# Kernel tuning notes

Hardware: AMD Instinct MI355X
Metric: run time of the kernel (lower is better)

Reference implementation:

```python
import jax, jax.numpy as jnp
import numpy as np

B, ES, HS, NL, NOUT, T = 16384, 64, 64, 3, 2, 128


def setup_inputs() -> dict:
    key = jax.random.key(0)
    ks = jax.random.split(key, 9)
    k = 1.0 / np.sqrt(HS)
    u = lambda kk, shape: jax.random.uniform(kk, shape, jnp.float32, -k, k)
    return {
        "agentFutureTrajEnc": jax.random.normal(ks[0], (B, ES), jnp.float32),
        "emb_w": u(ks[1], (ES, ES)),
        "emb_b": u(ks[2], (ES,)),
        "w_ih": u(ks[3], (NL, 3 * HS, ES)),
        "w_hh": u(ks[4], (NL, 3 * HS, HS)),
        "b_ih": u(ks[5], (NL, 3 * HS)),
        "b_hh": u(ks[6], (NL, 3 * HS)),
        "out_w": u(ks[7], (NOUT, HS)),
        "out_b": u(ks[8], (NOUT,)),
        "target_length": T,
        "batch_size": B,
    }


def _gru_cell(x, h, Wi, Wh, bi, bh):
    # PyTorch GRU cell math: gates ordered (r, z, n)
    gi = x @ Wi.T + bi            # (B, 3*hs)
    gh = h @ Wh.T + bh            # (B, 3*hs)
    ir, iz, inn = jnp.split(gi, 3, axis=-1)
    hr, hz, hn = jnp.split(gh, 3, axis=-1)
    r = jax.nn.sigmoid(ir + hr)
    z = jax.nn.sigmoid(iz + hz)
    n = jnp.tanh(inn + r * hn)
    return (1.0 - z) * n + z * h


def reference(agentFutureTrajEnc, emb_w, emb_b, w_ih, w_hh, b_ih, b_hh, out_w, out_b,
              target_length, batch_size):
    nl = w_ih.shape[0]
    # hidden initialized by repeating the encoding across layers: (nl, B, hs)
    h0 = jnp.broadcast_to(agentFutureTrajEnc[None], (nl,) + agentFutureTrajEnc.shape)

    def step(carry, _):
        x, h = carry                      # x: (B, es), h: (nl, B, hs)
        inp = x @ emb_w.T + emb_b         # embedding Linear(es->es)
        new_h = []
        for l in range(nl):               # small fixed layer loop
            hl = _gru_cell(inp, h[l], w_ih[l], w_hh[l], b_ih[l], b_hh[l])
            new_h.append(hl)
            inp = hl
        h = jnp.stack(new_h)              # (nl, B, hs)
        out = inp @ out_w.T + out_b       # (B, nout)
        return (h[-1], h), out            # next input is top-layer hidden

    _, outs = jax.lax.scan(step, (agentFutureTrajEnc, h0), None, length=target_length)
    return jnp.transpose(outs, (1, 0, 2))  # (B, T, nout)
```

## Files before the change

kernel.cpp:

```cpp
#include <hip/hip_runtime.h>


#define ESZ   64
#define HSZ   64
#define TLEN  128
#define NOUTC 2
#define LDW   72
#define TB16  (16*LDW)
#define L2E   1.44269504f

typedef _Float16 half8 __attribute__((ext_vector_type(8)));
typedef _Float16 half4 __attribute__((ext_vector_type(4)));
typedef float    floatx4 __attribute__((ext_vector_type(4)));
typedef float    floatx2 __attribute__((ext_vector_type(2)));

#define MFMA(a, b, c) __builtin_amdgcn_mfma_f32_16x16x32_f16((a), (b), (c), 0, 0, 0)

#define SBAR() asm volatile("s_waitcnt lgkmcnt(0)\n\ts_barrier" ::: "memory")

__global__ __launch_bounds__(768, 3) void gru_pipe(
    const float* __restrict__ enc,
    const float* __restrict__ emb_w,
    const float* __restrict__ emb_b,
    const float* __restrict__ w_ih,
    const float* __restrict__ w_hh,
    const float* __restrict__ b_ih,
    const float* __restrict__ b_hh,
    const float* __restrict__ out_w,
    const float* __restrict__ out_b,
    float* __restrict__ out)
{
    __shared__ _Float16 s_hl[3 * 4 * 2 * TB16];
    __shared__ float    s_btmp[3 * 64];

    const int tid  = threadIdx.x;
    const int wave = tid >> 6, lane = tid & 63;
    const int l = wave >> 2, g = wave & 3;
    const int q = lane >> 4, c = lane & 15;
    const int u  = (g << 4) | c;
    const int u4 = (g << 4) | (q << 2);
    const long wgbase = (long)blockIdx.x * 64;

    if (tid < 512) {
        const int row = tid >> 3, k0 = (tid & 7) << 3;
        const int j = row >> 4, rr = row & 15;
        const float* p = enc + (wgbase + row) * ESZ + k0;
        floatx4 s0 = *(const floatx4*)p;
        floatx4 s1 = *(const floatx4*)(p + 4);
        half8 v;
        #pragma unroll
        for (int x = 0; x < 4; ++x) { v[x] = (_Float16)s0[x]; v[4 + x] = (_Float16)s1[x]; }
        #pragma unroll
        for (int ly = 0; ly < 3; ++ly)
            *(half8*)&s_hl[((ly * 4 + j) * 2 + 1) * TB16 + rr * LDW + k0] = v;
    }

    auto ldw8s = [&](const float* p, float sc) {
        floatx4 a = *(const floatx4*)p, b = *(const floatx4*)(p + 4);
        half8 v;
        #pragma unroll
        for (int x = 0; x < 4; ++x) { v[x] = (_Float16)(a[x] * sc); v[4 + x] = (_Float16)(b[x] * sc); }
        return v;
    };
    half8 fR[4], fZ[4], fNi[2], fNh[2], fO[2];
    fO[0] = fO[1] = half8{};
    if (l == 0) {
        const float* wi = w_ih;
        const float* wh = w_hh;
        floatx4 aR[4], aZ[4], aN[4];
        #pragma unroll
        for (int x = 0; x < 4; ++x) { aR[x] = {0,0,0,0}; aZ[x] = {0,0,0,0}; aN[x] = {0,0,0,0}; }
        float bR = 0.f, bZ = 0.f, bN = 0.f;
        for (int k4 = 0; k4 < 64; k4 += 4) {
            floatx4 wr4 = *(const floatx4*)(wi + (u) * 64 + k4);
            floatx4 wz4 = *(const floatx4*)(wi + (64 + u) * 64 + k4);
            floatx4 wn4 = *(const floatx4*)(wi + (128 + u) * 64 + k4);
            floatx4 be4 = *(const floatx4*)(emb_b + k4);
            #pragma unroll
            for (int kk = 0; kk < 4; ++kk) {
                const float* er = emb_w + (k4 + kk) * 64;
                floatx4 e0 = *(const floatx4*)(er + q * 8);
                floatx4 e1 = *(const floatx4*)(er + q * 8 + 4);
                floatx4 e2 = *(const floatx4*)(er + 32 + q * 8);
                floatx4 e3 = *(const floatx4*)(er + 32 + q * 8 + 4);
                const float wr = wr4[kk], wz = wz4[kk], wn = wn4[kk];
                aR[0] += wr * e0; aR[1] += wr * e1; aR[2] += wr * e2; aR[3] += wr * e3;
                aZ[0] += wz * e0; aZ[1] += wz * e1; aZ[2] += wz * e2; aZ[3] += wz * e3;
                aN[0] += wn * e0; aN[1] += wn * e1; aN[2] += wn * e2; aN[3] += wn * e3;
                bR += wr * be4[kk]; bZ += wz * be4[kk]; bN += wn * be4[kk];
            }
        }
        #pragma unroll
        for (int x = 0; x < 4; ++x) {
            fR[0][x] = (_Float16)(-L2E * aR[0][x]);   fR[0][4 + x] = (_Float16)(-L2E * aR[1][x]);
            fR[1][x] = (_Float16)(-L2E * aR[2][x]);   fR[1][4 + x] = (_Float16)(-L2E * aR[3][x]);
            fZ[0][x] = (_Float16)(-L2E * aZ[0][x]);   fZ[0][4 + x] = (_Float16)(-L2E * aZ[1][x]);
            fZ[1][x] = (_Float16)(-L2E * aZ[2][x]);   fZ[1][4 + x] = (_Float16)(-L2E * aZ[3][x]);
            fNi[0][x] = (_Float16)(2*L2E * aN[0][x]); fNi[0][4 + x] = (_Float16)(2*L2E * aN[1][x]);
            fNi[1][x] = (_Float16)(2*L2E * aN[2][x]); fNi[1][4 + x] = (_Float16)(2*L2E * aN[3][x]);
        }
        fR[2]  = ldw8s(wh + (u) * 64 + q * 8, -L2E);        fR[3]  = ldw8s(wh + (u) * 64 + 32 + q * 8, -L2E);
        fZ[2]  = ldw8s(wh + (64 + u) * 64 + q * 8, -L2E);   fZ[3]  = ldw8s(wh + (64 + u) * 64 + 32 + q * 8, -L2E);
        fNh[0] = ldw8s(wh + (128 + u) * 64 + q * 8, 2*L2E); fNh[1] = ldw8s(wh + (128 + u) * 64 + 32 + q * 8, 2*L2E);
        if (q == 0) {
            s_btmp[u] = bR; s_btmp[64 + u] = bZ; s_btmp[128 + u] = bN;
        }
        const int oc = (c < NOUTC) ? c : 0;
        fO[0] = ldw8s(out_w + oc * 64 + q * 8, 1.f);
        fO[1] = ldw8s(out_w + oc * 64 + 32 + q * 8, 1.f);
    } else {
        const float* wi = w_ih + l * 3 * HSZ * ESZ;
        const float* wh = w_hh + l * 3 * HSZ * ESZ;
        fR[0]  = ldw8s(wi + (u) * 64 + q * 8, -L2E);        fR[1]  = ldw8s(wi + (u) * 64 + 32 + q * 8, -L2E);
        fR[2]  = ldw8s(wh + (u) * 64 + q * 8, -L2E);        fR[3]  = ldw8s(wh + (u) * 64 + 32 + q * 8, -L2E);
        fZ[0]  = ldw8s(wi + (64 + u) * 64 + q * 8, -L2E);   fZ[1]  = ldw8s(wi + (64 + u) * 64 + 32 + q * 8, -L2E);
        fZ[2]  = ldw8s(wh + (64 + u) * 64 + q * 8, -L2E);   fZ[3]  = ldw8s(wh + (64 + u) * 64 + 32 + q * 8, -L2E);
        fNi[0] = ldw8s(wi + (128 + u) * 64 + q * 8, 2*L2E); fNi[1] = ldw8s(wi + (128 + u) * 64 + 32 + q * 8, 2*L2E);
        fNh[0] = ldw8s(wh + (128 + u) * 64 + q * 8, 2*L2E); fNh[1] = ldw8s(wh + (128 + u) * 64 + 32 + q * 8, 2*L2E);
    }
    __syncthreads();

    floatx4 bR4, bZ4, bNi4, bNh4;
    if (l == 0) {
        #pragma unroll
        for (int i = 0; i < 4; ++i) {
            bR4[i]  = -L2E * (s_btmp[u4 + i] + b_ih[u4 + i] + b_hh[u4 + i]);
            bZ4[i]  = -L2E * (s_btmp[64 + u4 + i] + b_ih[64 + u4 + i] + b_hh[64 + u4 + i]);
            bNi4[i] = 2.f * L2E * (s_btmp[128 + u4 + i] + b_ih[128 + u4 + i]);
            bNh4[i] = 2.f * L2E * b_hh[128 + u4 + i];
        }
    } else {
        const int b0 = l * 192;
        floatx4 bi0 = *(const floatx4*)(b_ih + b0 + u4),       bh0 = *(const floatx4*)(b_hh + b0 + u4);
        floatx4 bi1 = *(const floatx4*)(b_ih + b0 + 64 + u4),  bh1 = *(const floatx4*)(b_hh + b0 + 64 + u4);
        floatx4 bi2 = *(const floatx4*)(b_ih + b0 + 128 + u4), bh2 = *(const floatx4*)(b_hh + b0 + 128 + u4);
        #pragma unroll
        for (int i = 0; i < 4; ++i) {
            bR4[i]  = -L2E * (bi0[i] + bh0[i]);
            bZ4[i]  = -L2E * (bi1[i] + bh1[i]);
            bNi4[i] = 2.f * L2E * bi2[i];
            bNh4[i] = 2.f * L2E * bh2[i];
        }
    }
    const float ob0 = out_b[0], ob1 = out_b[1];

    floatx4 ca0 = *(const floatx4*)(enc + (wgbase +  0 + c) * 64 + u4);
    floatx4 ca1 = *(const floatx4*)(enc + (wgbase + 16 + c) * 64 + u4);
    floatx4 ca2 = *(const floatx4*)(enc + (wgbase + 32 + c) * 64 + u4);
    floatx4 ca3 = *(const floatx4*)(enc + (wgbase + 48 + c) * 64 + u4);

    const int ar = c * LDW + (q << 3);

    auto visit = [&](const int ll, const int j, floatx4& cs, const int t,
                     const int parw) {
        const _Float16* hb = s_hl + ((ll * 4 + j) * 2 + (parw ^ 1)) * TB16;
        const _Float16* xb = (ll == 0) ? s_hl + ((8 + j) * 2 + (parw ^ 1)) * TB16
                                       : s_hl + (((ll - 1) * 4 + j) * 2 + parw) * TB16;
        half8 ah0 = *(const half8*)(hb + ar);
        half8 ah1 = *(const half8*)(hb + ar + 32);
        half8 bx0 = *(const half8*)(xb + ar);
        half8 bx1 = *(const half8*)(xb + ar + 32);
        floatx4 accr = bR4, accz = bZ4, accnh = bNh4;
        accr  = MFMA(fR[2], ah0, accr);   accr  = MFMA(fR[3], ah1, accr);
        accz  = MFMA(fZ[2], ah0, accz);   accz  = MFMA(fZ[3], ah1, accz);
        accnh = MFMA(fNh[0], ah0, accnh); accnh = MFMA(fNh[1], ah1, accnh);
        accr = MFMA(fR[0], bx0, accr); accr = MFMA(fR[1], bx1, accr);
        accz = MFMA(fZ[0], bx0, accz); accz = MFMA(fZ[1], bx1, accz);
        floatx4 accni = bNi4;
        accni = MFMA(fNi[0], bx0, accni); accni = MFMA(fNi[1], bx1, accni);
        _Float16* hw = s_hl + ((ll * 4 + j) * 2 + parw) * TB16 + c * LDW + u4;
        half4 hv4; floatx4 hnew;
        #pragma unroll
        for (int i = 0; i < 4; ++i) {
            const float r  = __builtin_amdgcn_rcpf(1.f + __builtin_amdgcn_exp2f(accr[i]));
            const float z  = __builtin_amdgcn_rcpf(1.f + __builtin_amdgcn_exp2f(accz[i]));
            const float a  = accni[i] + r * accnh[i];
            const float n  = 1.f - 2.f * __builtin_amdgcn_rcpf(1.f + __builtin_amdgcn_exp2f(a));
            const float hv = n + z * (cs[i] - n);
            hnew[i] = hv; hv4[i] = (_Float16)hv;
        }
        *(half4*)hw = hv4;
        cs = hnew;
        if (ll == 0 && g == j && t >= 1) {
            floatx4 oa = {ob0, ob1, 0.f, 0.f};
            oa = MFMA(fO[0], bx0, oa);
            oa = MFMA(fO[1], bx1, oa);
            if (q == 0) {
                const long row = wgbase + j * 16 + c;
                *(floatx2*)(out + (row * TLEN + (t - 1)) * NOUTC) = floatx2{oa[0], oa[1]};
            }
        }
    };

    for (int s4 = 0; s4 < TLEN; s4 += 2) {
        if (l == 0)      visit(0, 0, ca0, s4, 0);
        else if (l == 1) { if (s4) visit(1, 3, ca3, s4 - 1, 1); }
        else             { if (s4) visit(2, 2, ca2, s4 - 1, 1); }
        SBAR();
        if (l == 0)      visit(0, 1, ca1, s4, 0);
        else if (l == 1) visit(1, 0, ca0, s4, 0);
        else             { if (s4) visit(2, 3, ca3, s4 - 1, 1); }
        SBAR();
        if (l == 0)      visit(0, 2, ca2, s4, 0);
        else if (l == 1) visit(1, 1, ca1, s4, 0);
        else             visit(2, 0, ca0, s4, 0);
        SBAR();
        if (l == 0)      visit(0, 3, ca3, s4, 0);
        else if (l == 1) visit(1, 2, ca2, s4, 0);
        else             visit(2, 1, ca1, s4, 0);
        SBAR();
        if (l == 0)      visit(0, 0, ca0, s4 + 1, 1);
        else if (l == 1) visit(1, 3, ca3, s4, 0);
        else             visit(2, 2, ca2, s4, 0);
        SBAR();
        if (l == 0)      visit(0, 1, ca1, s4 + 1, 1);
        else if (l == 1) visit(1, 0, ca0, s4 + 1, 1);
        else             visit(2, 3, ca3, s4, 0);
        SBAR();
        if (l == 0)      visit(0, 2, ca2, s4 + 1, 1);
        else if (l == 1) visit(1, 1, ca1, s4 + 1, 1);
        else             visit(2, 0, ca0, s4 + 1, 1);
        SBAR();
        if (l == 0)      visit(0, 3, ca3, s4 + 1, 1);
        else if (l == 1) visit(1, 2, ca2, s4 + 1, 1);
        else             visit(2, 1, ca1, s4 + 1, 1);
        SBAR();
    }
    if (l == 1)      visit(1, 3, ca3, TLEN - 1, 1);
    else if (l == 2) visit(2, 2, ca2, TLEN - 1, 1);
    SBAR();
    if (l == 2)      visit(2, 3, ca3, TLEN - 1, 1);
    SBAR();

    if (l == 0) {
        const _Float16* xb = s_hl + ((8 + g) * 2 + 1) * TB16;
        half8 bx0 = *(const half8*)(xb + ar), bx1 = *(const half8*)(xb + ar + 32);
        floatx4 oa = {ob0, ob1, 0.f, 0.f};
        oa = MFMA(fO[0], bx0, oa);
        oa = MFMA(fO[1], bx1, oa);
        if (q == 0) {
            const long row = wgbase + g * 16 + c;
            *(floatx2*)(out + (row * TLEN + 127) * NOUTC) = floatx2{oa[0], oa[1]};
        }
    }
}

extern "C" void kernel_launch(void* const* d_in, const int* in_sizes, int n_in,
                              void* d_out, int out_size, void* d_ws, size_t ws_size,
                              hipStream_t stream) {
    (void)in_sizes; (void)n_in; (void)d_ws; (void)ws_size; (void)out_size;
    const int grid = 16384 / 64;
    gru_pipe<<<grid, 768, 0, stream>>>(
        (const float*)d_in[0],
        (const float*)d_in[1],
        (const float*)d_in[2],
        (const float*)d_in[3],
        (const float*)d_in[4],
        (const float*)d_in[5],
        (const float*)d_in[6],
        (const float*)d_in[7],
        (const float*)d_in[8],
        (float*)d_out);
}
```

Baseline: 453.6 us.

## Add dedicated output wavegroup, prefetch next hidden tile, share sigmoid reciprocal

The block grows from 12 to 16 waves, and the new fourth wave group computes the output projection that layer-0 waves used to do inline. Each layer stage now prefetches the hidden-state fragments for its next visit into registers before running the current step's MFMAs, hiding LDS latency across barriers. The r and z sigmoids share a single reciprocal of the product of their denominators, saving one rcp per element. The cost is more waves per block (launch bounds raised to 1024, 4), extra register pressure from the double-buffered fragments, and slightly different rounding in the gate computation.

```diff
diff --git a/kernel.cpp b/kernel.cpp
--- a/kernel.cpp
+++ b/kernel.cpp
@@ -18,7 +18,7 @@
 
 #define SBAR() asm volatile("s_waitcnt lgkmcnt(0)\n\ts_barrier" ::: "memory")
 
-__global__ __launch_bounds__(768, 3) void gru_pipe(
+__global__ __launch_bounds__(1024, 4) void gru_pipe(
     const float* __restrict__ enc,
     const float* __restrict__ emb_w,
     const float* __restrict__ emb_b,
@@ -63,7 +63,6 @@
         return v;
     };
     half8 fR[4], fZ[4], fNi[2], fNh[2], fO[2];
-    fO[0] = fO[1] = half8{};
     if (l == 0) {
         const float* wi = w_ih;
         const float* wh = w_hh;
@@ -105,10 +104,7 @@
         if (q == 0) {
             s_btmp[u] = bR; s_btmp[64 + u] = bZ; s_btmp[128 + u] = bN;
         }
-        const int oc = (c < NOUTC) ? c : 0;
-        fO[0] = ldw8s(out_w + oc * 64 + q * 8, 1.f);
-        fO[1] = ldw8s(out_w + oc * 64 + 32 + q * 8, 1.f);
-    } else {
+    } else if (l < 3) {
         const float* wi = w_ih + l * 3 * HSZ * ESZ;
         const float* wh = w_hh + l * 3 * HSZ * ESZ;
         fR[0]  = ldw8s(wi + (u) * 64 + q * 8, -L2E);        fR[1]  = ldw8s(wi + (u) * 64 + 32 + q * 8, -L2E);
@@ -117,6 +113,10 @@
         fZ[2]  = ldw8s(wh + (64 + u) * 64 + q * 8, -L2E);   fZ[3]  = ldw8s(wh + (64 + u) * 64 + 32 + q * 8, -L2E);
         fNi[0] = ldw8s(wi + (128 + u) * 64 + q * 8, 2*L2E); fNi[1] = ldw8s(wi + (128 + u) * 64 + 32 + q * 8, 2*L2E);
         fNh[0] = ldw8s(wh + (128 + u) * 64 + q * 8, 2*L2E); fNh[1] = ldw8s(wh + (128 + u) * 64 + 32 + q * 8, 2*L2E);
+    } else {
+        const int oc = (c < NOUTC) ? c : 0;
+        fO[0] = ldw8s(out_w + oc * 64 + q * 8, 1.f);
+        fO[1] = ldw8s(out_w + oc * 64 + 32 + q * 8, 1.f);
     }
     __syncthreads();
 
@@ -129,7 +129,7 @@
             bNi4[i] = 2.f * L2E * (s_btmp[128 + u4 + i] + b_ih[128 + u4 + i]);
             bNh4[i] = 2.f * L2E * b_hh[128 + u4 + i];
         }
-    } else {
+    } else if (l < 3) {
         const int b0 = l * 192;
         floatx4 bi0 = *(const floatx4*)(b_ih + b0 + u4),       bh0 = *(const floatx4*)(b_hh + b0 + u4);
         floatx4 bi1 = *(const floatx4*)(b_ih + b0 + 64 + u4),  bh1 = *(const floatx4*)(b_hh + b0 + 64 + u4);
@@ -151,98 +151,127 @@
 
     const int ar = c * LDW + (q << 3);
 
-    auto visit = [&](const int ll, const int j, floatx4& cs, const int t,
-                     const int parw) {
-        const _Float16* hb = s_hl + ((ll * 4 + j) * 2 + (parw ^ 1)) * TB16;
-        const _Float16* xb = (ll == 0) ? s_hl + ((8 + j) * 2 + (parw ^ 1)) * TB16
-                                       : s_hl + (((ll - 1) * 4 + j) * 2 + parw) * TB16;
-        half8 ah0 = *(const half8*)(hb + ar);
-        half8 ah1 = *(const half8*)(hb + ar + 32);
-        half8 bx0 = *(const half8*)(xb + ar);
-        half8 bx1 = *(const half8*)(xb + ar + 32);
-        floatx4 accr = bR4, accz = bZ4, accnh = bNh4;
-        accr  = MFMA(fR[2], ah0, accr);   accr  = MFMA(fR[3], ah1, accr);
-        accz  = MFMA(fZ[2], ah0, accz);   accz  = MFMA(fZ[3], ah1, accz);
-        accnh = MFMA(fNh[0], ah0, accnh); accnh = MFMA(fNh[1], ah1, accnh);
-        accr = MFMA(fR[0], bx0, accr); accr = MFMA(fR[1], bx1, accr);
-        accz = MFMA(fZ[0], bx0, accz); accz = MFMA(fZ[1], bx1, accz);
-        floatx4 accni = bNi4;
-        accni = MFMA(fNi[0], bx0, accni); accni = MFMA(fNi[1], bx1, accni);
-        _Float16* hw = s_hl + ((ll * 4 + j) * 2 + parw) * TB16 + c * LDW + u4;
-        half4 hv4; floatx4 hnew;
-        #pragma unroll
-        for (int i = 0; i < 4; ++i) {
-            const float r  = __builtin_amdgcn_rcpf(1.f + __builtin_amdgcn_exp2f(accr[i]));
-            const float z  = __builtin_amdgcn_rcpf(1.f + __builtin_amdgcn_exp2f(accz[i]));
-            const float a  = accni[i] + r * accnh[i];
-            const float n  = 1.f - 2.f * __builtin_amdgcn_rcpf(1.f + __builtin_amdgcn_exp2f(a));
-            const float hv = n + z * (cs[i] - n);
-            hnew[i] = hv; hv4[i] = (_Float16)hv;
-        }
-        *(half4*)hw = hv4;
-        cs = hnew;
-        if (ll == 0 && g == j && t >= 1) {
-            floatx4 oa = {ob0, ob1, 0.f, 0.f};
-            oa = MFMA(fO[0], bx0, oa);
-            oa = MFMA(fO[1], bx1, oa);
-            if (q == 0) {
-                const long row = wgbase + j * 16 + c;
-                *(floatx2*)(out + (row * TLEN + (t - 1)) * NOUTC) = floatx2{oa[0], oa[1]};
+    auto stageL = [&](const int ll, const int j, const int parw, const bool valid,
+                      half8& cah0, half8& cah1,
+                      half8& pah0, half8& pah1,
+                      const int nj, const int npw,
+                      floatx4& cs) {
+        half8 bx0, bx1;
+        if (valid) {
+            const _Float16* xb = (ll == 0) ? s_hl + ((8 + j) * 2 + (parw ^ 1)) * TB16
+                                           : s_hl + (((ll - 1) * 4 + j) * 2 + parw) * TB16;
+            bx0 = *(const half8*)(xb + ar);
+            bx1 = *(const half8*)(xb + ar + 32);
+        }
+        {
+            const _Float16* nhb = s_hl + ((ll * 4 + nj) * 2 + (npw ^ 1)) * TB16;
+            pah0 = *(const half8*)(nhb + ar);
+            pah1 = *(const half8*)(nhb + ar + 32);
+        }
+        if (valid) {
+            floatx4 accr = bR4, accz = bZ4, accnh = bNh4;
+            accr  = MFMA(fR[2], cah0, accr);   accr  = MFMA(fR[3], cah1, accr);
+            accz  = MFMA(fZ[2], cah0, accz);   accz  = MFMA(fZ[3], cah1, accz);
+            accnh = MFMA(fNh[0], cah0, accnh); accnh = MFMA(fNh[1], cah1, accnh);
+            accr = MFMA(fR[0], bx0, accr); accr = MFMA(fR[1], bx1, accr);
+            accz = MFMA(fZ[0], bx0, accz); accz = MFMA(fZ[1], bx1, accz);
+            floatx4 accni = bNi4;
+            accni = MFMA(fNi[0], bx0, accni); accni = MFMA(fNi[1], bx1, accni);
+            _Float16* hw = s_hl + ((ll * 4 + j) * 2 + parw) * TB16 + c * LDW + u4;
+            half4 hv4; floatx4 hnew;
+            #pragma unroll
+            for (int i = 0; i < 4; ++i) {
+                const float er = __builtin_amdgcn_exp2f(accr[i]);
+                const float ez = __builtin_amdgcn_exp2f(accz[i]);
+                const float pr = 1.f + er, pz = 1.f + ez;
+                const float qq = __builtin_amdgcn_rcpf(pr * pz);
+                const float rr = qq * pz;
+                const float zz = qq * pr;
+                const float a  = accni[i] + rr * accnh[i];
+                const float n  = 1.f - 2.f * __builtin_amdgcn_rcpf(1.f + __builtin_amdgcn_exp2f(a));
+                const float hv = n + zz * (cs[i] - n);
+                hnew[i] = hv; hv4[i] = (_Float16)hv;
             }
+            *(half4*)hw = hv4;
+            cs = hnew;
         }
     };
 
+    auto visO = [&](const int j, const int t, const int parw) {
+        if (g != j) return;
+        const _Float16* xb = s_hl + ((8 + j) * 2 + parw) * TB16;
+        half8 b0 = *(const half8*)(xb + ar);
+        half8 b1 = *(const half8*)(xb + ar + 32);
+        floatx4 oa = {ob0, ob1, 0.f, 0.f};
+        oa = MFMA(fO[0], b0, oa);
+        oa = MFMA(fO[1], b1, oa);
+        if (q == 0) {
+            const long row = wgbase + j * 16 + c;
+            *(floatx2*)(out + (row * TLEN + t) * NOUTC) = floatx2{oa[0], oa[1]};
+        }
+    };
+
+    half8 eh0, eh1, oh0, oh1;
+    if (l < 3) {
+        const int j0 = (l == 0) ? 0 : (l == 1) ? 3 : 2;
+        const int p0 = (l == 0) ? 1 : 0;
+        const _Float16* phb = s_hl + ((l * 4 + j0) * 2 + p0) * TB16;
+        eh0 = *(const half8*)(phb + ar);
+        eh1 = *(const half8*)(phb + ar + 32);
+    }
+
     for (int s4 = 0; s4 < TLEN; s4 += 2) {
-        if (l == 0)      visit(0, 0, ca0, s4, 0);
-        else if (l == 1) { if (s4) visit(1, 3, ca3, s4 - 1, 1); }
-        else             { if (s4) visit(2, 2, ca2, s4 - 1, 1); }
-        SBAR();
-        if (l == 0)      visit(0, 1, ca1, s4, 0);
-        else if (l == 1) visit(1, 0, ca0, s4, 0);
-        else             { if (s4) visit(2, 3, ca3, s4 - 1, 1); }
-        SBAR();
-        if (l == 0)      visit(0, 2, ca2, s4, 0);
-        else if (l == 1) visit(1, 1, ca1, s4, 0);
-        else             visit(2, 0, ca0, s4, 0);
-        SBAR();
-        if (l == 0)      visit(0, 3, ca3, s4, 0);
-        else if (l == 1) visit(1, 2, ca2, s4, 0);
-        else             visit(2, 1, ca1, s4, 0);
-        SBAR();
-        if (l == 0)      visit(0, 0, ca0, s4 + 1, 1);
-        else if (l == 1) visit(1, 3, ca3, s4, 0);
-        else             visit(2, 2, ca2, s4, 0);
-        SBAR();
-        if (l == 0)      visit(0, 1, ca1, s4 + 1, 1);
-        else if (l == 1) visit(1, 0, ca0, s4 + 1, 1);
-        else             visit(2, 3, ca3, s4, 0);
-        SBAR();
-        if (l == 0)      visit(0, 2, ca2, s4 + 1, 1);
-        else if (l == 1) visit(1, 1, ca1, s4 + 1, 1);
-        else             visit(2, 0, ca0, s4 + 1, 1);
-        SBAR();
-        if (l == 0)      visit(0, 3, ca3, s4 + 1, 1);
-        else if (l == 1) visit(1, 2, ca2, s4 + 1, 1);
-        else             visit(2, 1, ca1, s4 + 1, 1);
-        SBAR();
-    }
-    if (l == 1)      visit(1, 3, ca3, TLEN - 1, 1);
-    else if (l == 2) visit(2, 2, ca2, TLEN - 1, 1);
+        const bool vv = (s4 != 0);
+        if (l == 0)      stageL(0, 0, 0, true, eh0, eh1, oh0, oh1, 1, 0, ca0);
+        else if (l == 1) stageL(1, 3, 1, vv,   eh0, eh1, oh0, oh1, 0, 0, ca3);
+        else if (l == 2) stageL(2, 2, 1, vv,   eh0, eh1, oh0, oh1, 3, 1, ca2);
+        else if (vv)     visO(1, s4 - 1, 1);
+        SBAR();
+        if (l == 0)      stageL(0, 1, 0, true, oh0, oh1, eh0, eh1, 2, 0, ca1);
+        else if (l == 1) stageL(1, 0, 0, true, oh0, oh1, eh0, eh1, 1, 0, ca0);
+        else if (l == 2) stageL(2, 3, 1, vv,   oh0, oh1, eh0, eh1, 0, 0, ca3);
+        else if (vv)     visO(2, s4 - 1, 1);
+        SBAR();
+        if (l == 0)      stageL(0, 2, 0, true, eh0, eh1, oh0, oh1, 3, 0, ca2);
+        else if (l == 1) stageL(1, 1, 0, true, eh0, eh1, oh0, oh1, 2, 0, ca1);
+        else if (l == 2) stageL(2, 0, 0, true, eh0, eh1, oh0, oh1, 1, 0, ca0);
+        else if (vv)     visO(3, s4 - 1, 1);
+        SBAR();
+        if (l == 0)      stageL(0, 3, 0, true, oh0, oh1, eh0, eh1, 0, 1, ca3);
+        else if (l == 1) stageL(1, 2, 0, true, oh0, oh1, eh0, eh1, 3, 0, ca2);
+        else if (l == 2) stageL(2, 1, 0, true, oh0, oh1, eh0, eh1, 2, 0, ca1);
+        else             visO(0, s4, 0);
+        SBAR();
+        if (l == 0)      stageL(0, 0, 1, true, eh0, eh1, oh0, oh1, 1, 1, ca0);
+        else if (l == 1) stageL(1, 3, 0, true, eh0, eh1, oh0, oh1, 0, 1, ca3);
+        else if (l == 2) stageL(2, 2, 0, true, eh0, eh1, oh0, oh1, 3, 0, ca2);
+        else             visO(1, s4, 0);
+        SBAR();
+        if (l == 0)      stageL(0, 1, 1, true, oh0, oh1, eh0, eh1, 2, 1, ca1);
+        else if (l == 1) stageL(1, 0, 1, true, oh0, oh1, eh0, eh1, 1, 1, ca0);
+        else if (l == 2) stageL(2, 3, 0, true, oh0, oh1, eh0, eh1, 0, 1, ca3);
+        else             visO(2, s4, 0);
+        SBAR();
+        if (l == 0)      stageL(0, 2, 1, true, eh0, eh1, oh0, oh1, 3, 1, ca2);
+        else if (l == 1) stageL(1, 1, 1, true, eh0, eh1, oh0, oh1, 2, 1, ca1);
+        else if (l == 2) stageL(2, 0, 1, true, eh0, eh1, oh0, oh1, 1, 1, ca0);
+        else             visO(3, s4, 0);
+        SBAR();
+        if (l == 0)      stageL(0, 3, 1, true, oh0, oh1, eh0, eh1, 0, 0, ca3);
+        else if (l == 1) stageL(1, 2, 1, true, oh0, oh1, eh0, eh1, 3, 1, ca2);
+        else if (l == 2) stageL(2, 1, 1, true, oh0, oh1, eh0, eh1, 2, 1, ca1);
+        else             visO(0, s4 + 1, 1);
+        SBAR();
+    }
+
+    if (l == 1)      stageL(1, 3, 1, true, eh0, eh1, oh0, oh1, 0, 0, ca3);
+    else if (l == 2) stageL(2, 2, 1, true, eh0, eh1, oh0, oh1, 3, 1, ca2);
+    else if (l == 3) visO(1, TLEN - 1, 1);
     SBAR();
-    if (l == 2)      visit(2, 3, ca3, TLEN - 1, 1);
+    if (l == 2)      stageL(2, 3, 1, true, oh0, oh1, eh0, eh1, 0, 0, ca3);
+    else if (l == 3) visO(2, TLEN - 1, 1);
     SBAR();
-
-    if (l == 0) {
-        const _Float16* xb = s_hl + ((8 + g) * 2 + 1) * TB16;
-        half8 bx0 = *(const half8*)(xb + ar), bx1 = *(const half8*)(xb + ar + 32);
-        floatx4 oa = {ob0, ob1, 0.f, 0.f};
-        oa = MFMA(fO[0], bx0, oa);
-        oa = MFMA(fO[1], bx1, oa);
-        if (q == 0) {
-            const long row = wgbase + g * 16 + c;
-            *(floatx2*)(out + (row * TLEN + 127) * NOUTC) = floatx2{oa[0], oa[1]};
-        }
-    }
+    if (l == 3) visO(3, TLEN - 1, 1);
 }
 
 extern "C" void kernel_launch(void* const* d_in, const int* in_sizes, int n_in,
@@ -250,7 +279,7 @@
                               hipStream_t stream) {
     (void)in_sizes; (void)n_in; (void)d_ws; (void)ws_size; (void)out_size;
     const int grid = 16384 / 64;
-    gru_pipe<<<grid, 768, 0, stream>>>(
+    gru_pipe<<<grid, 1024, 0, stream>>>(
         (const float*)d_in[0],
         (const float*)d_in[1],
         (const float*)d_in[2],
```

Result: slower. 1.039 ms (+129.0%).

## Software-pipeline recurrent h-matmuls one slot ahead and fuse sigmoid reciprocals

Applied to the files above, without the earlier changes.

Restructures the wavefront GRU schedule so each slot computes the hidden-state MFMAs for its next visit ahead of time, carrying the accumulators across the barrier. Only the input-dependent MFMAs and the nonlinearity stay on the critical path after each barrier. It also raises wave priority around the MFMA issue and merges the r and z sigmoid reciprocals into a single rcp plus multiplies. The cost is more live accumulator registers, and the prefetched h reads depend on the next-slot indices being encoded correctly.

```diff
diff --git a/kernel.cpp b/kernel.cpp
--- a/kernel.cpp
+++ b/kernel.cpp
@@ -151,85 +151,120 @@
 
     const int ar = c * LDW + (q << 3);
 
-    auto visit = [&](const int ll, const int j, floatx4& cs, const int t,
-                     const int parw) {
-        const _Float16* hb = s_hl + ((ll * 4 + j) * 2 + (parw ^ 1)) * TB16;
-        const _Float16* xb = (ll == 0) ? s_hl + ((8 + j) * 2 + (parw ^ 1)) * TB16
-                                       : s_hl + (((ll - 1) * 4 + j) * 2 + parw) * TB16;
+    floatx4 accrC = bR4, acczC = bZ4, accnhC = bNh4;
+
+    auto slotF = [&](const int ll, const int j, floatx4& cs, const int t,
+                     const int parw, const bool valid,
+                     const int nj, const int nparw) {
+        __builtin_amdgcn_s_setprio(1);
+        half8 bx0, bx1;
+        if (valid) {
+            const _Float16* xb = (ll == 0) ? s_hl + ((8 + j) * 2 + (parw ^ 1)) * TB16
+                                           : s_hl + (((ll - 1) * 4 + j) * 2 + parw) * TB16;
+            bx0 = *(const half8*)(xb + ar);
+            bx1 = *(const half8*)(xb + ar + 32);
+        }
+        const _Float16* hb = s_hl + ((ll * 4 + nj) * 2 + (nparw ^ 1)) * TB16;
         half8 ah0 = *(const half8*)(hb + ar);
         half8 ah1 = *(const half8*)(hb + ar + 32);
-        half8 bx0 = *(const half8*)(xb + ar);
-        half8 bx1 = *(const half8*)(xb + ar + 32);
-        floatx4 accr = bR4, accz = bZ4, accnh = bNh4;
-        accr  = MFMA(fR[2], ah0, accr);   accr  = MFMA(fR[3], ah1, accr);
-        accz  = MFMA(fZ[2], ah0, accz);   accz  = MFMA(fZ[3], ah1, accz);
-        accnh = MFMA(fNh[0], ah0, accnh); accnh = MFMA(fNh[1], ah1, accnh);
-        accr = MFMA(fR[0], bx0, accr); accr = MFMA(fR[1], bx1, accr);
-        accz = MFMA(fZ[0], bx0, accz); accz = MFMA(fZ[1], bx1, accz);
-        floatx4 accni = bNi4;
-        accni = MFMA(fNi[0], bx0, accni); accni = MFMA(fNi[1], bx1, accni);
-        _Float16* hw = s_hl + ((ll * 4 + j) * 2 + parw) * TB16 + c * LDW + u4;
-        half4 hv4; floatx4 hnew;
-        #pragma unroll
-        for (int i = 0; i < 4; ++i) {
-            const float r  = __builtin_amdgcn_rcpf(1.f + __builtin_amdgcn_exp2f(accr[i]));
-            const float z  = __builtin_amdgcn_rcpf(1.f + __builtin_amdgcn_exp2f(accz[i]));
-            const float a  = accni[i] + r * accnh[i];
-            const float n  = 1.f - 2.f * __builtin_amdgcn_rcpf(1.f + __builtin_amdgcn_exp2f(a));
-            const float hv = n + z * (cs[i] - n);
-            hnew[i] = hv; hv4[i] = (_Float16)hv;
-        }
-        *(half4*)hw = hv4;
-        cs = hnew;
-        if (ll == 0 && g == j && t >= 1) {
-            floatx4 oa = {ob0, ob1, 0.f, 0.f};
-            oa = MFMA(fO[0], bx0, oa);
-            oa = MFMA(fO[1], bx1, oa);
-            if (q == 0) {
-                const long row = wgbase + j * 16 + c;
-                *(floatx2*)(out + (row * TLEN + (t - 1)) * NOUTC) = floatx2{oa[0], oa[1]};
+        floatx4 accr = accrC, accz = acczC, accnh = accnhC;
+        {
+            floatx4 r = bR4, z = bZ4, nh = bNh4;
+            r  = MFMA(fR[2], ah0, r);   r  = MFMA(fR[3], ah1, r);
+            z  = MFMA(fZ[2], ah0, z);   z  = MFMA(fZ[3], ah1, z);
+            nh = MFMA(fNh[0], ah0, nh); nh = MFMA(fNh[1], ah1, nh);
+            accrC = r; acczC = z; accnhC = nh;
+        }
+        if (valid) {
+            accr = MFMA(fR[0], bx0, accr); accr = MFMA(fR[1], bx1, accr);
+            accz = MFMA(fZ[0], bx0, accz); accz = MFMA(fZ[1], bx1, accz);
+            floatx4 accni = bNi4;
+            accni = MFMA(fNi[0], bx0, accni); accni = MFMA(fNi[1], bx1, accni);
+            __builtin_amdgcn_s_setprio(0);
+            _Float16* hw = s_hl + ((ll * 4 + j) * 2 + parw) * TB16 + c * LDW + u4;
+            half4 hv4; floatx4 hnew;
+            #pragma unroll
+            for (int i = 0; i < 4; ++i) {
+                const float er = __builtin_amdgcn_exp2f(accr[i]);
+                const float ez = __builtin_amdgcn_exp2f(accz[i]);
+                const float pr = 1.f + er, pz = 1.f + ez;
+                const float qq = __builtin_amdgcn_rcpf(pr * pz);
+                const float rr = qq * pz;
+                const float zz = qq * pr;
+                const float a  = accni[i] + rr * accnh[i];
+                const float n  = 1.f - 2.f * __builtin_amdgcn_rcpf(1.f + __builtin_amdgcn_exp2f(a));
+                const float hv = n + zz * (cs[i] - n);
+                hnew[i] = hv; hv4[i] = (_Float16)hv;
             }
+            *(half4*)hw = hv4;
+            cs = hnew;
+            if (ll == 0 && g == j && t >= 1) {
+                floatx4 oa = {ob0, ob1, 0.f, 0.f};
+                oa = MFMA(fO[0], bx0, oa);
+                oa = MFMA(fO[1], bx1, oa);
+                if (q == 0) {
+                    const long row = wgbase + j * 16 + c;
+                    *(floatx2*)(out + (row * TLEN + (t - 1)) * NOUTC) = floatx2{oa[0], oa[1]};
+                }
+            }
+        } else {
+            __builtin_amdgcn_s_setprio(0);
         }
     };
 
-    for (int s4 = 0; s4 < TLEN; s4 += 2) {
-        if (l == 0)      visit(0, 0, ca0, s4, 0);
-        else if (l == 1) { if (s4) visit(1, 3, ca3, s4 - 1, 1); }
-        else             { if (s4) visit(2, 2, ca2, s4 - 1, 1); }
-        SBAR();
-        if (l == 0)      visit(0, 1, ca1, s4, 0);
-        else if (l == 1) visit(1, 0, ca0, s4, 0);
-        else             { if (s4) visit(2, 3, ca3, s4 - 1, 1); }
-        SBAR();
-        if (l == 0)      visit(0, 2, ca2, s4, 0);
-        else if (l == 1) visit(1, 1, ca1, s4, 0);
-        else             visit(2, 0, ca0, s4, 0);
-        SBAR();
-        if (l == 0)      visit(0, 3, ca3, s4, 0);
-        else if (l == 1) visit(1, 2, ca2, s4, 0);
-        else             visit(2, 1, ca1, s4, 0);
-        SBAR();
-        if (l == 0)      visit(0, 0, ca0, s4 + 1, 1);
-        else if (l == 1) visit(1, 3, ca3, s4, 0);
-        else             visit(2, 2, ca2, s4, 0);
-        SBAR();
-        if (l == 0)      visit(0, 1, ca1, s4 + 1, 1);
-        else if (l == 1) visit(1, 0, ca0, s4 + 1, 1);
-        else             visit(2, 3, ca3, s4, 0);
-        SBAR();
-        if (l == 0)      visit(0, 2, ca2, s4 + 1, 1);
-        else if (l == 1) visit(1, 1, ca1, s4 + 1, 1);
-        else             visit(2, 0, ca0, s4 + 1, 1);
-        SBAR();
-        if (l == 0)      visit(0, 3, ca3, s4 + 1, 1);
-        else if (l == 1) visit(1, 2, ca2, s4 + 1, 1);
-        else             visit(2, 1, ca1, s4 + 1, 1);
-        SBAR();
-    }
-    if (l == 1)      visit(1, 3, ca3, TLEN - 1, 1);
-    else if (l == 2) visit(2, 2, ca2, TLEN - 1, 1);
+    {
+        const int j0 = (l == 0) ? 0 : (l == 1) ? 3 : 2;
+        const int p0 = (l == 0) ? 0 : 1;
+        const _Float16* hb = s_hl + ((l * 4 + j0) * 2 + (p0 ^ 1)) * TB16;
+        half8 ah0 = *(const half8*)(hb + ar);
+        half8 ah1 = *(const half8*)(hb + ar + 32);
+        floatx4 r = bR4, z = bZ4, nh = bNh4;
+        r  = MFMA(fR[2], ah0, r);   r  = MFMA(fR[3], ah1, r);
+        z  = MFMA(fZ[2], ah0, z);   z  = MFMA(fZ[3], ah1, z);
+        nh = MFMA(fNh[0], ah0, nh); nh = MFMA(fNh[1], ah1, nh);
+        accrC = r; acczC = z; accnhC = nh;
+    }
+
+    for (int t = 0; t < TLEN; t += 2) {
+        const bool vv = (t != 0);
+        if (l == 0)      slotF(0, 0, ca0, t, 0, true, 1, 0);
+        else if (l == 1) slotF(1, 3, ca3, t - 1, 1, vv, 0, 0);
+        else             slotF(2, 2, ca2, t - 1, 1, vv, 3, 1);
+        SBAR();
+        if (l == 0)      slotF(0, 1, ca1, t, 0, true, 2, 0);
+        else if (l == 1) slotF(1, 0, ca0, t, 0, true, 1, 0);
+        else             slotF(2, 3, ca3, t - 1, 1, vv, 0, 0);
+        SBAR();
+        if (l == 0)      slotF(0, 2, ca2, t, 0, true, 3, 0);
+        else if (l == 1) slotF(1, 1, ca1, t, 0, true, 2, 0);
+        else             slotF(2, 0, ca0, t, 0, true, 1, 0);
+        SBAR();
+        if (l == 0)      slotF(0, 3, ca3, t, 0, true, 0, 1);
+        else if (l == 1) slotF(1, 2, ca2, t, 0, true, 3, 0);
+        else             slotF(2, 1, ca1, t, 0, true, 2, 0);
+        SBAR();
+        if (l == 0)      slotF(0, 0, ca0, t + 1, 1, true, 1, 1);
+        else if (l == 1) slotF(1, 3, ca3, t, 0, true, 0, 1);
+        else             slotF(2, 2, ca2, t, 0, true, 3, 0);
+        SBAR();
+        if (l == 0)      slotF(0, 1, ca1, t + 1, 1, true, 2, 1);
+        else if (l == 1) slotF(1, 0, ca0, t + 1, 1, true, 1, 1);
+        else             slotF(2, 3, ca3, t, 0, true, 0, 1);
+        SBAR();
+        if (l == 0)      slotF(0, 2, ca2, t + 1, 1, true, 3, 1);
+        else if (l == 1) slotF(1, 1, ca1, t + 1, 1, true, 2, 1);
+        else             slotF(2, 0, ca0, t + 1, 1, true, 1, 1);
+        SBAR();
+        if (l == 0)      slotF(0, 3, ca3, t + 1, 1, true, 0, 0);
+        else if (l == 1) slotF(1, 2, ca2, t + 1, 1, true, 3, 1);
+        else             slotF(2, 1, ca1, t + 1, 1, true, 2, 1);
+        SBAR();
+    }
+
+    if (l == 1)      slotF(1, 3, ca3, TLEN - 1, 1, true, 0, 0);
+    else if (l == 2) slotF(2, 2, ca2, TLEN - 1, 1, true, 3, 1);
     SBAR();
-    if (l == 2)      visit(2, 3, ca3, TLEN - 1, 1);
+    if (l == 2)      slotF(2, 3, ca3, TLEN - 1, 1, true, 0, 0);
     SBAR();
 
     if (l == 0) {
```

New measurement: 477.3 us. 1.05x slower.
